# Performance work log

Measured on AMD Instinct MI355X. Metric: run time of the kernel, lower is better.

## Reference

```python
import jax, jax.numpy as jnp
import numpy as np

BITS = 256      # bits per token
HEADS = 8       # num voting heads
NPOS = 4        # n_position_bits for RELATIVE encoder (binary code of distance)
MAXD = 8        # max_distance of position encoder
NBPN = 12       # n_bits_per_neuron = min(similarity_bits, 12)
SEQ = 2048      # number of tokens
SIM = 2 * BITS + NPOS  # similarity_bits


def setup_inputs() -> dict:
    key = jax.random.key(0)
    k1, k2, k3 = jax.random.split(key, 3)
    tokens = jax.random.randint(k1, (SEQ, BITS), 0, 2, dtype=jnp.int32)
    head_idx = jax.random.randint(k2, (HEADS, NBPN), 0, SIM, dtype=jnp.int32)
    # RAM table contents: one bit (0/1) per address per head (trained lookup table)
    table = jax.random.bernoulli(k3, 0.5, (HEADS, 2 ** NBPN)).astype(jnp.float32)
    return {"tokens": tokens, "head_idx": head_idx, "table": table}


def reference(tokens, head_idx, table):
    S, B = tokens.shape
    H, K = head_idx.shape
    w = (2 ** jnp.arange(K)).astype(jnp.int32)  # slot weight 2^k per selected bit

    # relative-distance binary code table for distances 0..MAXD  -> (MAXD+1, NPOS)
    d_vals = jnp.arange(MAXD + 1)
    rel_bits = ((d_vals[:, None] >> jnp.arange(NPOS)[None, :]) & 1).astype(jnp.int32)

    # which source each selected bit position comes from within cat([query,key,rel])
    mask_q = (head_idx < B)
    mask_k = (head_idx >= B) & (head_idx < 2 * B)
    mask_r = head_idx >= 2 * B

    qg = tokens[:, jnp.clip(head_idx, 0, B - 1)]            # (S, H, K)
    kg = tokens[:, jnp.clip(head_idx - B, 0, B - 1)]        # (S, H, K)
    rg = rel_bits[:, jnp.clip(head_idx - 2 * B, 0, NPOS - 1)]  # (MAXD+1, H, K)

    # separable address contributions (query / key / relative distance)
    Aq = jnp.einsum('shk,hk->sh', qg, (mask_q * w).astype(jnp.int32))  # (S, H)
    Ak = jnp.einsum('shk,hk->sh', kg, (mask_k * w).astype(jnp.int32))  # (S, H)
    Ar = jnp.einsum('dhk,hk->dh', rg, (mask_r * w).astype(jnp.int32))  # (MAXD+1, H)

    i = jnp.arange(S)
    dist = jnp.clip(i[:, None] - i[None, :], 0, MAXD)        # (S, S)
    addr = Aq[:, None, :] + Ak[None, :, :] + Ar[dist]        # (S, S, H)

    head_votes = table[jnp.arange(H)[None, None, :], addr]   # (S, S, H)
    tril = (i[None, :] <= i[:, None]).astype(table.dtype)    # j > i gets vote 0
    votes = head_votes.sum(-1) * tril                        # (S, S)

    thr = H // 2
    attended = (votes >= thr).astype(table.dtype)            # (S, S)
    included = attended.sum(-1)                              # (S,)

    tok_f = tokens.astype(table.dtype)
    # XOR of selected tokens == per-bit parity of their sum
    parity = jnp.mod(attended @ tok_f, 2.0)                  # (S, B)
    # fallback: first token with max vote when nothing crossed the threshold
    fallback = tok_f[jnp.argmax(votes, axis=-1)]             # (S, B)
    return jnp.where((included > 0)[:, None], parity, fallback)
```

## Files before the change

### kernel.cpp

```cpp
#include <hip/hip_runtime.h>
#include <stdint.h>

#define SEQ   2048
#define BITS  256
#define HEADS 8
#define NPOS  4
#define MAXD  8
#define NBPN  12
#define TBLN  4096
#define TBLW  64

typedef unsigned long long u64;
typedef unsigned int       u32;
typedef unsigned short     u16;

#define OFF_TBL    0
#define OFF_PACKED 4096
#define OFF_AQ     (4096 + 65536)
#define OFF_AK     (4096 + 65536 + 32768)
#define OFF_AR     (4096 + 65536 + 65536)

__global__ void pack_table_kernel(const float* __restrict__ table,
                                  u64* __restrict__ tblbits) {
    int t = blockIdx.x * blockDim.x + threadIdx.x;
    if (t >= HEADS * TBLW) return;
    const float* p = table + t * 64;
    u64 bits = 0;
    #pragma unroll
    for (int b = 0; b < 64; ++b) bits |= (u64)(p[b] != 0.0f) << b;
    tblbits[t] = bits;
}

__global__ void pack_tokens_kernel(const int* __restrict__ tokens,
                                   u64* __restrict__ packed) {
    int t = blockIdx.x * blockDim.x + threadIdx.x;
    const int* p = tokens + t * 64;
    u64 bits = 0;
    #pragma unroll
    for (int b = 0; b < 64; ++b) bits |= (u64)(p[b] & 1) << b;
    packed[t] = bits;
}

__global__ void addr_parts_kernel(const int* __restrict__ tokens,
                                  const int* __restrict__ head_idx,
                                  u16* __restrict__ Aq, u16* __restrict__ Ak,
                                  u16* __restrict__ Ar) {
    int t = blockIdx.x * blockDim.x + threadIdx.x;
    int s = t >> 3, h = t & 7;
    const int* hi  = head_idx + h * NBPN;
    const int* tok = tokens + s * BITS;
    int aq = 0, ak = 0;
    #pragma unroll
    for (int k = 0; k < NBPN; ++k) {
        int idx = hi[k];
        if (idx < BITS)            aq += tok[idx] << k;
        else if (idx < 2 * BITS)   ak += tok[idx - BITS] << k;
    }
    Aq[t] = (u16)aq;
    Ak[t] = (u16)ak;
    if (t < (MAXD + 1) * HEADS) {
        int d = t / HEADS, hh = t % HEADS;
        const int* hi2 = head_idx + hh * NBPN;
        int ar = 0;
        #pragma unroll
        for (int k = 0; k < NBPN; ++k) {
            int idx = hi2[k];
            if (idx >= 2 * BITS) {
                int p = idx - 2 * BITS;
                ar += ((d >> p) & 1) << k;
            }
        }
        Ar[t] = (u16)ar;
    }
}

__device__ inline u64 shfl_down_u64(u64 x, int o) {
    u32 lo = (u32)x, hi = (u32)(x >> 32);
    lo = __shfl_down(lo, o, 64);
    hi = __shfl_down(hi, o, 64);
    return ((u64)hi << 32) | lo;
}

__global__ __launch_bounds__(256) void row_kernel(
        const u64* __restrict__ tblbits, const u64* __restrict__ packed,
        const u16* __restrict__ Aq, const u16* __restrict__ Ak,
        const u16* __restrict__ Ar, float* __restrict__ out) {

    __shared__ u64 tbl[HEADS * TBLW];
    __shared__ u16 aqar[MAXD + 1][HEADS];
    __shared__ u64 r_acc[4][4];
    __shared__ int r_inc[4];
    __shared__ u64 r_key[4];
    __shared__ u64 f_acc[4];
    __shared__ int f_inc;
    __shared__ int f_bestj;

    const int i   = blockIdx.x;
    const int tid = threadIdx.x;

    tbl[tid]       = tblbits[tid];
    tbl[tid + 256] = tblbits[tid + 256];
    if (tid < (MAXD + 1) * HEADS) {
        int h = tid % HEADS;
        aqar[tid / HEADS][h] = (u16)(Aq[i * HEADS + h] + Ar[tid]);
    }
    __syncthreads();

    u64 acc0 = 0, acc1 = 0, acc2 = 0, acc3 = 0;
    int inc = 0;
    u64 bestkey = 0;

    for (int j = tid; j <= i; j += 256) {
        int dist = i - j; if (dist > MAXD) dist = MAXD;
        const uint4 akv = *(const uint4*)(Ak + j * HEADS);
        u32 wv[4] = { akv.x, akv.y, akv.z, akv.w };
        int votes = 0;
        #pragma unroll
        for (int h = 0; h < 8; ++h) {
            u32 ak_h = (wv[h >> 1] >> ((h & 1) * 16)) & 0xFFFFu;
            u32 addr = (u32)aqar[dist][h] + ak_h;
            votes += (int)((tbl[h * TBLW + (addr >> 6)] >> (addr & 63)) & 1ull);
        }
        int att = (votes >= HEADS / 2) ? 1 : 0;
        u64 m = (u64)0 - (u64)att;
        const u64* pj = packed + j * 4;
        acc0 ^= pj[0] & m; acc1 ^= pj[1] & m;
        acc2 ^= pj[2] & m; acc3 ^= pj[3] & m;
        inc += att;
        u64 key = ((u64)(votes + 1) << 32) | (u64)(0x7FFFFFFF - j);
        if (key > bestkey) bestkey = key;
    }

    #pragma unroll
    for (int o = 32; o > 0; o >>= 1) {
        acc0 ^= shfl_down_u64(acc0, o);
        acc1 ^= shfl_down_u64(acc1, o);
        acc2 ^= shfl_down_u64(acc2, o);
        acc3 ^= shfl_down_u64(acc3, o);
        inc  += __shfl_down(inc, o, 64);
        u64 k2 = shfl_down_u64(bestkey, o);
        if (k2 > bestkey) bestkey = k2;
    }
    int wave = tid >> 6;
    if ((tid & 63) == 0) {
        r_acc[wave][0] = acc0; r_acc[wave][1] = acc1;
        r_acc[wave][2] = acc2; r_acc[wave][3] = acc3;
        r_inc[wave] = inc; r_key[wave] = bestkey;
    }
    __syncthreads();
    if (tid == 0) {
        u64 a0 = 0, a1 = 0, a2 = 0, a3 = 0, bk = 0; int ic = 0;
        #pragma unroll
        for (int w = 0; w < 4; ++w) {
            a0 ^= r_acc[w][0]; a1 ^= r_acc[w][1];
            a2 ^= r_acc[w][2]; a3 ^= r_acc[w][3];
            ic += r_inc[w];
            if (r_key[w] > bk) bk = r_key[w];
        }
        f_acc[0] = a0; f_acc[1] = a1; f_acc[2] = a2; f_acc[3] = a3;
        f_inc = ic;
        f_bestj = 0x7FFFFFFF - (int)(bk & 0xFFFFFFFFu);
    }
    __syncthreads();

    int b = tid;
    u64 wordv = (f_inc > 0) ? f_acc[b >> 6]
                            : packed[f_bestj * 4 + (b >> 6)];
    out[i * BITS + b] = (float)((wordv >> (b & 63)) & 1ull);
}

extern "C" void kernel_launch(void* const* d_in, const int* in_sizes, int n_in,
                              void* d_out, int out_size, void* d_ws, size_t ws_size,
                              hipStream_t stream) {
    const int*   tokens   = (const int*)d_in[0];
    const int*   head_idx = (const int*)d_in[1];
    const float* table    = (const float*)d_in[2];
    float*       out      = (float*)d_out;
    char*        ws       = (char*)d_ws;

    u64* tblbits = (u64*)(ws + OFF_TBL);
    u64* packed  = (u64*)(ws + OFF_PACKED);
    u16* Aq      = (u16*)(ws + OFF_AQ);
    u16* Ak      = (u16*)(ws + OFF_AK);
    u16* Ar      = (u16*)(ws + OFF_AR);

    pack_table_kernel <<<2,  256, 0, stream>>>(table, tblbits);
    pack_tokens_kernel<<<32, 256, 0, stream>>>(tokens, packed);
    addr_parts_kernel <<<64, 256, 0, stream>>>(tokens, head_idx, Aq, Ak, Ar);
    row_kernel        <<<SEQ, 256, 0, stream>>>(tblbits, packed, Aq, Ak, Ar, out);
}
```

Measured before the change: 80.43 us.

## Merge prep kernels with ballot packing and shrink row kernel to 128 threads

```diff
diff --git a/kernel.cpp b/kernel.cpp
--- a/kernel.cpp
+++ b/kernel.cpp
@@ -7,8 +7,6 @@
 #define NPOS  4
 #define MAXD  8
 #define NBPN  12
-#define TBLN  4096
-#define TBLW  64
 
 typedef unsigned long long u64;
 typedef unsigned int       u32;
@@ -20,57 +18,45 @@
 #define OFF_AK     (4096 + 65536 + 32768)
 #define OFF_AR     (4096 + 65536 + 65536)
 
-__global__ void pack_table_kernel(const float* __restrict__ table,
-                                  u64* __restrict__ tblbits) {
-    int t = blockIdx.x * blockDim.x + threadIdx.x;
-    if (t >= HEADS * TBLW) return;
-    const float* p = table + t * 64;
-    u64 bits = 0;
-    #pragma unroll
-    for (int b = 0; b < 64; ++b) bits |= (u64)(p[b] != 0.0f) << b;
-    tblbits[t] = bits;
-}
-
-__global__ void pack_tokens_kernel(const int* __restrict__ tokens,
-                                   u64* __restrict__ packed) {
-    int t = blockIdx.x * blockDim.x + threadIdx.x;
-    const int* p = tokens + t * 64;
-    u64 bits = 0;
-    #pragma unroll
-    for (int b = 0; b < 64; ++b) bits |= (u64)(p[b] & 1) << b;
-    packed[t] = bits;
-}
-
-__global__ void addr_parts_kernel(const int* __restrict__ tokens,
-                                  const int* __restrict__ head_idx,
-                                  u16* __restrict__ Aq, u16* __restrict__ Ak,
-                                  u16* __restrict__ Ar) {
-    int t = blockIdx.x * blockDim.x + threadIdx.x;
-    int s = t >> 3, h = t & 7;
-    const int* hi  = head_idx + h * NBPN;
-    const int* tok = tokens + s * BITS;
-    int aq = 0, ak = 0;
-    #pragma unroll
-    for (int k = 0; k < NBPN; ++k) {
-        int idx = hi[k];
-        if (idx < BITS)            aq += tok[idx] << k;
-        else if (idx < 2 * BITS)   ak += tok[idx - BITS] << k;
-    }
-    Aq[t] = (u16)aq;
-    Ak[t] = (u16)ak;
-    if (t < (MAXD + 1) * HEADS) {
-        int d = t / HEADS, hh = t % HEADS;
-        const int* hi2 = head_idx + hh * NBPN;
-        int ar = 0;
+__global__ __launch_bounds__(256) void prep_kernel(
+        const int* __restrict__ tokens, const int* __restrict__ head_idx,
+        const float* __restrict__ table,
+        u64* __restrict__ tblbits, u64* __restrict__ packed,
+        u16* __restrict__ Aq, u16* __restrict__ Ak, u16* __restrict__ Ar) {
+    const int bid = blockIdx.x, tid = threadIdx.x;
+    if (bid < 2048) {
+        int t = bid * 256 + tid;
+        u64 m = __ballot(tokens[t] & 1);
+        if ((tid & 63) == 0) packed[t >> 6] = m;
+    } else if (bid < 2048 + 128) {
+        int t = (bid - 2048) * 256 + tid;
+        u64 m = __ballot(table[t] != 0.0f);
+        if ((tid & 63) == 0) tblbits[t >> 6] = m;
+    } else {
+        int t = (bid - 2176) * 256 + tid;
+        int s = t >> 3, h = t & 7;
+        const int* hi  = head_idx + h * NBPN;
+        const int* tok = tokens + s * BITS;
+        int aq = 0, ak = 0;
         #pragma unroll
         for (int k = 0; k < NBPN; ++k) {
-            int idx = hi2[k];
-            if (idx >= 2 * BITS) {
-                int p = idx - 2 * BITS;
-                ar += ((d >> p) & 1) << k;
+            int idx = hi[k];
+            if (idx < BITS)          aq += tok[idx] << k;
+            else if (idx < 2 * BITS) ak += tok[idx - BITS] << k;
+        }
+        Aq[t] = (u16)aq;
+        Ak[t] = (u16)ak;
+        if (t < (MAXD + 1) * HEADS) {
+            int d = t / HEADS, hh = t % HEADS;
+            const int* hi2 = head_idx + hh * NBPN;
+            int ar = 0;
+            #pragma unroll
+            for (int k = 0; k < NBPN; ++k) {
+                int idx = hi2[k];
+                if (idx >= 2 * BITS) ar += ((d >> (idx - 2 * BITS)) & 1) << k;
             }
+            Ar[t] = (u16)ar;
         }
-        Ar[t] = (u16)ar;
     }
 }
 
@@ -81,51 +67,63 @@
     return ((u64)hi << 32) | lo;
 }
 
-__global__ __launch_bounds__(256) void row_kernel(
+__global__ __launch_bounds__(128) void row_kernel(
         const u64* __restrict__ tblbits, const u64* __restrict__ packed,
         const u16* __restrict__ Aq, const u16* __restrict__ Ak,
         const u16* __restrict__ Ar, float* __restrict__ out) {
 
-    __shared__ u64 tbl[HEADS * TBLW];
+    __shared__ u32 tbl[HEADS * 128];
     __shared__ u16 aqar[MAXD + 1][HEADS];
-    __shared__ u64 r_acc[4][4];
-    __shared__ int r_inc[4];
-    __shared__ u64 r_key[4];
-    __shared__ u64 f_acc[4];
-    __shared__ int f_inc;
-    __shared__ int f_bestj;
+    __shared__ u64 p_acc[2][4];
+    __shared__ int p_inc[2];
+    __shared__ u64 p_key[2];
 
     const int i   = blockIdx.x;
     const int tid = threadIdx.x;
 
-    tbl[tid]       = tblbits[tid];
-    tbl[tid + 256] = tblbits[tid + 256];
+    const u32* tb32 = (const u32*)tblbits;
+    #pragma unroll
+    for (int w = 0; w < 8; ++w) tbl[tid + w * 128] = tb32[tid + w * 128];
     if (tid < (MAXD + 1) * HEADS) {
-        int h = tid % HEADS;
-        aqar[tid / HEADS][h] = (u16)(Aq[i * HEADS + h] + Ar[tid]);
+        int h = tid & 7;
+        aqar[tid >> 3][h] = (u16)(Aq[i * HEADS + h] + Ar[tid]);
     }
     __syncthreads();
+
+    u32 a8[8];
+    #pragma unroll
+    for (int h = 0; h < 8; ++h) a8[h] = aqar[MAXD][h];
 
     u64 acc0 = 0, acc1 = 0, acc2 = 0, acc3 = 0;
     int inc = 0;
     u64 bestkey = 0;
 
-    for (int j = tid; j <= i; j += 256) {
-        int dist = i - j; if (dist > MAXD) dist = MAXD;
+    for (int j = tid; j <= i; j += 128) {
+        int dist = i - j;
         const uint4 akv = *(const uint4*)(Ak + j * HEADS);
-        u32 wv[4] = { akv.x, akv.y, akv.z, akv.w };
         int votes = 0;
-        #pragma unroll
-        for (int h = 0; h < 8; ++h) {
-            u32 ak_h = (wv[h >> 1] >> ((h & 1) * 16)) & 0xFFFFu;
-            u32 addr = (u32)aqar[dist][h] + ak_h;
-            votes += (int)((tbl[h * TBLW + (addr >> 6)] >> (addr & 63)) & 1ull);
+        if (__any(dist < MAXD)) {
+            #pragma unroll
+            for (int h = 0; h < 8; ++h) {
+                u32 ak_h = ((&akv.x)[h >> 1] >> ((h & 1) * 16)) & 0xFFFFu;
+                u32 base = (dist >= MAXD) ? a8[h] : (u32)aqar[dist][h];
+                u32 addr = base + ak_h;
+                votes += (int)((tbl[(h << 7) + (addr >> 5)] >> (addr & 31)) & 1u);
+            }
+        } else {
+            #pragma unroll
+            for (int h = 0; h < 8; ++h) {
+                u32 ak_h = ((&akv.x)[h >> 1] >> ((h & 1) * 16)) & 0xFFFFu;
+                u32 addr = a8[h] + ak_h;
+                votes += (int)((tbl[(h << 7) + (addr >> 5)] >> (addr & 31)) & 1u);
+            }
         }
         int att = (votes >= HEADS / 2) ? 1 : 0;
         u64 m = (u64)0 - (u64)att;
-        const u64* pj = packed + j * 4;
-        acc0 ^= pj[0] & m; acc1 ^= pj[1] & m;
-        acc2 ^= pj[2] & m; acc3 ^= pj[3] & m;
+        const ulonglong2* pj = (const ulonglong2*)(packed + j * 4);
+        ulonglong2 pA = pj[0], pB = pj[1];
+        acc0 ^= pA.x & m; acc1 ^= pA.y & m;
+        acc2 ^= pB.x & m; acc3 ^= pB.y & m;
         inc += att;
         u64 key = ((u64)(votes + 1) << 32) | (u64)(0x7FFFFFFF - j);
         if (key > bestkey) bestkey = key;
@@ -143,30 +141,32 @@
     }
     int wave = tid >> 6;
     if ((tid & 63) == 0) {
-        r_acc[wave][0] = acc0; r_acc[wave][1] = acc1;
-        r_acc[wave][2] = acc2; r_acc[wave][3] = acc3;
-        r_inc[wave] = inc; r_key[wave] = bestkey;
-    }
-    __syncthreads();
-    if (tid == 0) {
-        u64 a0 = 0, a1 = 0, a2 = 0, a3 = 0, bk = 0; int ic = 0;
-        #pragma unroll
-        for (int w = 0; w < 4; ++w) {
-            a0 ^= r_acc[w][0]; a1 ^= r_acc[w][1];
-            a2 ^= r_acc[w][2]; a3 ^= r_acc[w][3];
-            ic += r_inc[w];
-            if (r_key[w] > bk) bk = r_key[w];
-        }
-        f_acc[0] = a0; f_acc[1] = a1; f_acc[2] = a2; f_acc[3] = a3;
-        f_inc = ic;
-        f_bestj = 0x7FFFFFFF - (int)(bk & 0xFFFFFFFFu);
+        p_acc[wave][0] = acc0; p_acc[wave][1] = acc1;
+        p_acc[wave][2] = acc2; p_acc[wave][3] = acc3;
+        p_inc[wave] = inc; p_key[wave] = bestkey;
     }
     __syncthreads();
 
-    int b = tid;
-    u64 wordv = (f_inc > 0) ? f_acc[b >> 6]
-                            : packed[f_bestj * 4 + (b >> 6)];
-    out[i * BITS + b] = (float)((wordv >> (b & 63)) & 1ull);
+    u64 f0 = p_acc[0][0] ^ p_acc[1][0];
+    u64 f1 = p_acc[0][1] ^ p_acc[1][1];
+    u64 f2 = p_acc[0][2] ^ p_acc[1][2];
+    u64 f3 = p_acc[0][3] ^ p_acc[1][3];
+    int finc = p_inc[0] + p_inc[1];
+    u64 fk = (p_key[0] > p_key[1]) ? p_key[0] : p_key[1];
+
+    int b0  = tid * 2;
+    int wsel = tid >> 5;
+    u64 word;
+    if (finc > 0) {
+        word = (wsel < 2) ? (wsel == 0 ? f0 : f1) : (wsel == 2 ? f2 : f3);
+    } else {
+        int bestj = 0x7FFFFFFF - (int)(fk & 0xFFFFFFFFu);
+        word = packed[bestj * 4 + wsel];
+    }
+    int sh = b0 & 63;
+    float2 o2 = make_float2((float)((word >> sh) & 1ull),
+                            (float)((word >> (sh + 1)) & 1ull));
+    *(float2*)(out + i * BITS + b0) = o2;
 }
 
 extern "C" void kernel_launch(void* const* d_in, const int* in_sizes, int n_in,
@@ -184,8 +184,7 @@
     u16* Ak      = (u16*)(ws + OFF_AK);
     u16* Ar      = (u16*)(ws + OFF_AR);
 
-    pack_table_kernel <<<2,  256, 0, stream>>>(table, tblbits);
-    pack_tokens_kernel<<<32, 256, 0, stream>>>(tokens, packed);
-    addr_parts_kernel <<<64, 256, 0, stream>>>(tokens, head_idx, Aq, Ak, Ar);
-    row_kernel        <<<SEQ, 256, 0, stream>>>(tblbits, packed, Aq, Ak, Ar, out);
+    prep_kernel<<<2240, 256, 0, stream>>>(tokens, head_idx, table,
+                                          tblbits, packed, Aq, Ak, Ar);
+    row_kernel <<<SEQ, 128, 0, stream>>>(tblbits, packed, Aq, Ak, Ar, out);
 }
```

Result: faster. 76.43 us (-5.0%).
